# Performance work log

Measured on AMD Instinct MI355X. Metric: run time of the kernel, lower is better.

The kernel has to match this reference:

```python
import jax, jax.numpy as jnp
import numpy as np

NUM_BINS = 8
TAIL_BOUND = 3.0
MIN_V = 1e-3
MIN_DERIV = 1e-3


def _normalize(u):
    # softmax -> min-width floor -> cumsum -> pad left -> map to [-tail, tail]
    v = jax.nn.softmax(u, axis=-1)
    v = MIN_V + (1.0 - MIN_V * NUM_BINS) * v
    cum = jnp.cumsum(v, axis=-1)
    cum = jnp.pad(cum, [(0, 0)] * (cum.ndim - 1) + [(1, 0)])
    return (cum - 0.5) * 2.0 * TAIL_BOUND, v


def _rqs(x_dyn, u_w, u_h, u_d):
    # x_dyn: [B, D]; u_w/u_h: [B, D, K]; u_d: [B, D, K+1]
    cum_w, w = _normalize(u_w)
    cum_h, h = _normalize(u_h)
    d = jax.nn.softplus(u_d) + MIN_DERIV
    cum_w = cum_w.at[..., -1].add(1e-6)  # searchsorted eps on last edge

    idx = jnp.sum((x_dyn[..., None] >= cum_w).astype(jnp.int32), axis=-1) - 1
    idx = jnp.clip(idx, 0, NUM_BINS - 1)[..., None]  # [B, D, 1]

    take = lambda a, i: jnp.take_along_axis(a, i, axis=-1)[..., 0]
    cw, ww = take(cum_w, idx), take(w, idx)
    ch, hh = take(cum_h, idx), take(h, idx)
    di = jnp.clip(take(d, idx), MIN_DERIV, 1000.0)
    di1 = jnp.clip(take(d, idx + 1), MIN_DERIV, 1000.0)

    delta = hh / ww
    theta = jnp.clip((x_dyn - cw) / ww, 0.0, 1.0)
    t1m = theta * (1.0 - theta)
    num_term = di1 * theta ** 2 + delta * t1m
    den = jnp.maximum(delta + (di + di1 - 2.0 * delta) * t1m, 1e-6)
    spline_out = ch + delta * num_term / den * ww
    deriv_num = delta ** 2 * (di1 * theta ** 2 + 2.0 * delta * t1m + di * (1.0 - theta) ** 2)
    spline_logdet = jnp.log(jnp.maximum(deriv_num / den ** 2, 1e-12))

    in_range = (x_dyn >= -TAIL_BOUND) & (x_dyn <= TAIL_BOUND)
    out = jnp.where(in_range, spline_out, x_dyn)
    logdet = jnp.where(in_range, spline_logdet, 0.0)
    return out, logdet


def setup_inputs() -> dict:
    key = jax.random.key(0)
    ks = jax.random.split(key, 3)
    B, D, H = 32768, 128, 256
    total = 3 * NUM_BINS + 1
    x = jax.random.normal(ks[0], (B, D), dtype=jnp.float32)
    mask = (jnp.arange(D) % 2).astype(jnp.float32)
    W1 = jax.random.normal(ks[1], (D, H), dtype=jnp.float32) * (1.0 / np.sqrt(D))
    b1 = jnp.zeros((H,), dtype=jnp.float32)
    W2 = jax.random.normal(ks[2], (H, D * total), dtype=jnp.float32) * (1.0 / np.sqrt(H))
    b2 = jnp.zeros((D * total,), dtype=jnp.float32)
    return {"x": x, "mask": mask, "W1": W1, "b1": b1, "W2": W2, "b2": b2}


def reference(x, mask, W1, b1, W2, b2):
    B, D = x.shape
    total = 3 * NUM_BINS + 1
    x_static = x * mask
    x_dyn = x * (1.0 - mask)
    hidden = jax.nn.relu(x_static @ W1 + b1)
    params = (hidden @ W2 + b2).reshape(B, D, total)
    u_w = params[..., :NUM_BINS]
    u_h = params[..., NUM_BINS:2 * NUM_BINS]
    u_d = params[..., 2 * NUM_BINS:]
    new_dyn, logdet = _rqs(x_dyn, u_w, u_h, u_d)
    out = x_static + new_dyn * (1.0 - mask)
    log_det = jnp.sum(logdet * (1.0 - mask), axis=1)
    return out, log_det
```

## Files before the change

### kernel.cpp

```cpp
#include <hip/hip_runtime.h>
#include <hip/hip_bf16.h>
#include <stdint.h>


#define B_ROWS 32768
#define DDIM   128
#define HDIM   256
#define NPAD   2048
#define LOSCALE 2048.0f
#define INV_LOSCALE (1.0f / 2048.0f)

using f32x4 = __attribute__((ext_vector_type(4))) float;
using f16x8 = __attribute__((ext_vector_type(8))) _Float16;

__device__ __forceinline__ void gl_lds16(const void* g, void* l) {
    __builtin_amdgcn_global_load_lds(
        (__attribute__((address_space(1))) void*)(void*)g,
        (__attribute__((address_space(3))) void*)l, 16, 0, 0);
}

__device__ __forceinline__ float rcpf(float x) { return __builtin_amdgcn_rcpf(x); }

__device__ __forceinline__ float softplus_fast(float z) {
    return fmaxf(z, 0.0f) + __logf(1.0f + __expf(-fabsf(z)));
}

__device__ __forceinline__ void rqs(const float* P, float xv, float& o, float& l) {
    float ew[8], vw[8], edw[9];
    float mw = P[0];
    #pragma unroll
    for (int j = 1; j < 8; ++j) mw = fmaxf(mw, P[j]);
    float sw = 0.0f;
    #pragma unroll
    for (int j = 0; j < 8; ++j) { ew[j] = expf(P[j] - mw); sw += ew[j]; }
    float rsw = rcpf(sw);
    float cum = 0.0f;
    edw[0] = -3.0f;
    #pragma unroll
    for (int j = 0; j < 8; ++j) {
        vw[j] = 0.001f + 0.992f * (ew[j] * rsw);
        cum += vw[j];
        edw[j + 1] = (cum - 0.5f) * 6.0f;
    }
    edw[8] += 1e-6f;

    float eh[8], vh[8], edh[9];
    float mh = P[8];
    #pragma unroll
    for (int j = 1; j < 8; ++j) mh = fmaxf(mh, P[8 + j]);
    float sh = 0.0f;
    #pragma unroll
    for (int j = 0; j < 8; ++j) { eh[j] = expf(P[8 + j] - mh); sh += eh[j]; }
    float rsh = rcpf(sh);
    float cumh = 0.0f;
    edh[0] = -3.0f;
    #pragma unroll
    for (int j = 0; j < 8; ++j) {
        vh[j] = 0.001f + 0.992f * (eh[j] * rsh);
        cumh += vh[j];
        edh[j + 1] = (cumh - 0.5f) * 6.0f;
    }

    float dk[9];
    #pragma unroll
    for (int j = 0; j < 9; ++j) dk[j] = softplus_fast(P[16 + j]) + 0.001f;

    int idx = -1;
    #pragma unroll
    for (int j = 0; j < 9; ++j) idx += (xv >= edw[j]) ? 1 : 0;
    idx = min(max(idx, 0), 7);

    float cw = edw[0], ww = vw[0], ch = edh[0], hh = vh[0], di = dk[0], di1 = dk[1];
    #pragma unroll
    for (int j = 0; j < 8; ++j) {
        bool sel = (idx == j);
        cw  = sel ? edw[j]    : cw;
        ww  = sel ? vw[j]     : ww;
        ch  = sel ? edh[j]    : ch;
        hh  = sel ? vh[j]     : hh;
        di  = sel ? dk[j]     : di;
        di1 = sel ? dk[j + 1] : di1;
    }
    di  = fminf(fmaxf(di,  0.001f), 1000.0f);
    di1 = fminf(fmaxf(di1, 0.001f), 1000.0f);

    float rww   = rcpf(ww);
    float delta = hh * rww;
    float theta = fminf(fmaxf((xv - cw) * rww, 0.0f), 1.0f);
    float t1m   = theta * (1.0f - theta);
    float th2   = theta * theta;
    float omt   = 1.0f - theta;
    float num_term = di1 * th2 + delta * t1m;
    float den      = fmaxf(delta + (di + di1 - 2.0f * delta) * t1m, 1e-6f);
    float rden     = rcpf(den);
    float sp       = ch + delta * num_term * rden * ww;
    float dn       = (delta * delta) * (di1 * th2 + 2.0f * delta * t1m + di * (omt * omt));
    float ld       = __logf(fmaxf(dn * rden * rden, 1e-12f));

    bool inr = (xv >= -3.0f) && (xv <= 3.0f);
    o = inr ? sp : xv;
    l = inr ? ld : 0.0f;
}

__global__ __launch_bounds__(256, 4) void k1_hidden(const float* __restrict__ x,
                                                    const float* __restrict__ W1,
                                                    const float* __restrict__ b1,
                                                    _Float16* __restrict__ hid_hi,
                                                    _Float16* __restrict__ hid_lo,
                                                    float* __restrict__ out,
                                                    float* __restrict__ logdet) {
    __shared__ float xod[32][64];
    const int t  = threadIdx.x;
    const int rb = blockIdx.x * 32;
    #pragma unroll
    for (int u = 0; u < 8; ++u) {
        int idx = u * 256 + t;
        int r = idx >> 6, k = idx & 63;
        float2 v = *(const float2*)&x[(rb + r) * DDIM + 2 * k];
        xod[r][k] = v.y;
        *(float2*)&out[(rb + r) * DDIM + 2 * k] = v;
    }
    if (t < 32) logdet[rb + t] = 0.0f;
    __syncthreads();
    float acc[32];
    #pragma unroll
    for (int r = 0; r < 32; ++r) acc[r] = 0.0f;
    #pragma unroll 2
    for (int k = 0; k < 64; ++k) {
        float w = W1[(2 * k + 1) * HDIM + t];
        #pragma unroll
        for (int r = 0; r < 32; ++r) acc[r] += xod[r][k] * w;
    }
    float bias = b1[t];
    #pragma unroll
    for (int r = 0; r < 32; ++r) {
        float h = fmaxf(acc[r] + bias, 0.0f);
        _Float16 hi = (_Float16)h;
        hid_hi[(rb + r) * HDIM + t] = hi;
        hid_lo[(rb + r) * HDIM + t] = (_Float16)((h - (float)hi) * LOSCALE);
    }
}

__global__ __launch_bounds__(256) void k3_w2split(const float* __restrict__ W2,
                                                  _Float16* __restrict__ w2t_hi,
                                                  _Float16* __restrict__ w2t_lo) {
    int tid = blockIdx.x * 256 + threadIdx.x;
    int n  = tid >> 5;
    int kc = tid & 31;
    int de = n >> 5, j = n & 31;
    f16x8 vh, vl;
    #pragma unroll
    for (int i = 0; i < 8; ++i) {
        float v = (j < 25) ? W2[(size_t)(kc * 8 + i) * 3200 + 50 * de + j] : 0.0f;
        _Float16 h = (_Float16)v;
        vh[i] = h;
        vl[i] = (_Float16)((v - (float)h) * LOSCALE);
    }
    *(f16x8*)&w2t_hi[(size_t)n * HDIM + kc * 8] = vh;
    *(f16x8*)&w2t_lo[(size_t)n * HDIM + kc * 8] = vl;
}

__global__ __launch_bounds__(256, 2) void k2_mfma(
        const float* __restrict__ x,
        const _Float16* __restrict__ hid_hi, const _Float16* __restrict__ hid_lo,
        const _Float16* __restrict__ w2t_hi, const _Float16* __restrict__ w2t_lo,
        const float* __restrict__ b2,
        float* __restrict__ out, float* __restrict__ logdet) {
    __shared__ __align__(16) char smem[128 * 133 * 4];
    const int t    = threadIdx.x;
    const int lane = t & 63;
    const int wave = t >> 6;
    const int m0   = (wave & 1) * 64;
    const int n0   = (wave >> 1) * 64;
    const int row0 = blockIdx.y * 128;
    const int col0 = blockIdx.x * 128;

    f32x4 acc[4][4], acc2[4][4];
    #pragma unroll
    for (int i = 0; i < 4; ++i)
        #pragma unroll
        for (int j = 0; j < 4; ++j) {
            acc[i][j]  = (f32x4){0.f, 0.f, 0.f, 0.f};
            acc2[i][j] = (f32x4){0.f, 0.f, 0.f, 0.f};
        }

    for (int ks = 0; ks < 4; ++ks) {
        __syncthreads();
        #pragma unroll
        for (int call = 0; call < 4; ++call) {
            int g = call * 4 + wave;
            int s = g * 64 + lane;
            int r = s >> 3;
            int c = (s & 7) ^ (r & 7);
            int ke = ks * 64 + c * 8;
            char* ldsb = smem + g * 1024;
            gl_lds16(hid_hi + (size_t)(row0 + r) * HDIM + ke, ldsb);
            gl_lds16(hid_lo + (size_t)(row0 + r) * HDIM + ke, ldsb + 16384);
            gl_lds16(w2t_hi + (size_t)(col0 + r) * HDIM + ke, ldsb + 32768);
            gl_lds16(w2t_lo + (size_t)(col0 + r) * HDIM + ke, ldsb + 49152);
        }
        __syncthreads();
        #pragma unroll
        for (int kk = 0; kk < 2; ++kk) {
            int kc = kk * 4 + (lane >> 4);
            int sw = ((kc ^ (lane & 7)) << 4);
            f16x8 ah[4], al[4], bh[4], bl[4];
            #pragma unroll
            for (int i = 0; i < 4; ++i) {
                int oa = (m0 + i * 16 + (lane & 15)) * 128 + sw;
                ah[i] = *(const f16x8*)(smem + oa);
                al[i] = *(const f16x8*)(smem + 16384 + oa);
                int ob = (n0 + i * 16 + (lane & 15)) * 128 + sw;
                bh[i] = *(const f16x8*)(smem + 32768 + ob);
                bl[i] = *(const f16x8*)(smem + 49152 + ob);
            }
            #pragma unroll
            for (int mi = 0; mi < 4; ++mi)
                #pragma unroll
                for (int ni = 0; ni < 4; ++ni) {
                    acc[mi][ni]  = __builtin_amdgcn_mfma_f32_16x16x32_f16(ah[mi], bh[ni], acc[mi][ni],  0, 0, 0);
                    acc2[mi][ni] = __builtin_amdgcn_mfma_f32_16x16x32_f16(al[mi], bh[ni], acc2[mi][ni], 0, 0, 0);
                    acc2[mi][ni] = __builtin_amdgcn_mfma_f32_16x16x32_f16(ah[mi], bl[ni], acc2[mi][ni], 0, 0, 0);
                }
        }
    }

    __syncthreads();
    float* pf = (float*)smem;
    #pragma unroll
    for (int mi = 0; mi < 4; ++mi)
        #pragma unroll
        for (int ni = 0; ni < 4; ++ni)
            #pragma unroll
            for (int e = 0; e < 4; ++e) {
                int rl = m0 + mi * 16 + (lane >> 4) * 4 + e;
                int cl = n0 + ni * 16 + (lane & 15);
                pf[rl * 133 + cl] = acc[mi][ni][e] + acc2[mi][ni][e] * INV_LOSCALE;
            }
    __syncthreads();

    const int rl   = t & 127;
    const int rowg = blockIdx.y * 128 + rl;
    float ldsum = 0.0f;
    #pragma unroll
    for (int pp = 0; pp < 2; ++pp) {
        int deg = (t >> 7) + 2 * pp;
        int de  = blockIdx.x * 4 + deg;
        float xv = x[(size_t)rowg * DDIM + 2 * de];
        float P[25];
        #pragma unroll
        for (int j = 0; j < 25; ++j)
            P[j] = pf[rl * 133 + deg * 32 + j] + b2[50 * de + j];
        float o, l;
        rqs(P, xv, o, l);
        out[(size_t)rowg * DDIM + 2 * de] = o;
        ldsum += l;
    }
    atomicAdd(&logdet[rowg], ldsum);
}

extern "C" void kernel_launch(void* const* d_in, const int* in_sizes, int n_in,
                              void* d_out, int out_size, void* d_ws, size_t ws_size,
                              hipStream_t stream) {
    const float* x  = (const float*)d_in[0];
    const float* W1 = (const float*)d_in[2];
    const float* b1 = (const float*)d_in[3];
    const float* W2 = (const float*)d_in[4];
    const float* b2 = (const float*)d_in[5];

    float* out    = (float*)d_out;
    float* logdet = (float*)d_out + (size_t)B_ROWS * DDIM;

    _Float16* hid_hi = (_Float16*)d_ws;
    _Float16* hid_lo = hid_hi + (size_t)B_ROWS * HDIM;
    _Float16* w2t_hi = hid_lo + (size_t)B_ROWS * HDIM;
    _Float16* w2t_lo = w2t_hi + (size_t)NPAD * HDIM;

    k3_w2split<<<dim3(NPAD * 32 / 256), dim3(256), 0, stream>>>(W2, w2t_hi, w2t_lo);
    k1_hidden <<<dim3(B_ROWS / 32),     dim3(256), 0, stream>>>(x, W1, b1, hid_hi, hid_lo, out, logdet);
    k2_mfma   <<<dim3(NPAD / 128, B_ROWS / 128), dim3(256), 0, stream>>>(
        x, hid_hi, hid_lo, w2t_hi, w2t_lo, b2, out, logdet);
}
```

Measured before the change: 229.9 us.

## Pack W2 columns densely (5 dims per tile) and register-tile hidden GEMM

The W2 column layout changes from padding each dim's 25 params to 32 to packing 5 dims (125 columns) per 128-column tile. This shrinks the padded N dimension of the main MFMA GEMM from 2048 to 1664 columns and cuts wasted tensor work, and the epilogue is adjusted to process up to 5 dims per block over 3 passes. Separately, the first-layer kernel now uses a transposed LDS tile and an 8x4 register block per thread with float4 loads and vectorized half stores. The risk is an uneven epilogue, where the last pass only half-fills threads and the last tile has partial dims.

```diff
diff --git a/kernel.cpp b/kernel.cpp
--- a/kernel.cpp
+++ b/kernel.cpp
@@ -6,12 +6,13 @@
 #define B_ROWS 32768
 #define DDIM   128
 #define HDIM   256
-#define NPAD   2048
+#define NPACK  1664
 #define LOSCALE 2048.0f
 #define INV_LOSCALE (1.0f / 2048.0f)
 
 using f32x4 = __attribute__((ext_vector_type(4))) float;
 using f16x8 = __attribute__((ext_vector_type(8))) _Float16;
+using f16x4 = __attribute__((ext_vector_type(4))) _Float16;
 
 __device__ __forceinline__ void gl_lds16(const void* g, void* l) {
     __builtin_amdgcn_global_load_lds(
@@ -109,35 +110,56 @@
                                                     _Float16* __restrict__ hid_lo,
                                                     float* __restrict__ out,
                                                     float* __restrict__ logdet) {
-    __shared__ float xod[32][64];
+    __shared__ float xodT[64][36];
     const int t  = threadIdx.x;
     const int rb = blockIdx.x * 32;
+    const int cg = t & 63;
+    const int rg = t >> 6;
     #pragma unroll
     for (int u = 0; u < 8; ++u) {
         int idx = u * 256 + t;
         int r = idx >> 6, k = idx & 63;
         float2 v = *(const float2*)&x[(rb + r) * DDIM + 2 * k];
-        xod[r][k] = v.y;
+        xodT[k][r] = v.y;
         *(float2*)&out[(rb + r) * DDIM + 2 * k] = v;
     }
     if (t < 32) logdet[rb + t] = 0.0f;
     __syncthreads();
-    float acc[32];
-    #pragma unroll
-    for (int r = 0; r < 32; ++r) acc[r] = 0.0f;
-    #pragma unroll 2
+
+    float acc[8][4];
+    #pragma unroll
+    for (int r = 0; r < 8; ++r)
+        #pragma unroll
+        for (int c = 0; c < 4; ++c) acc[r][c] = 0.0f;
+
+    #pragma unroll 4
     for (int k = 0; k < 64; ++k) {
-        float w = W1[(2 * k + 1) * HDIM + t];
-        #pragma unroll
-        for (int r = 0; r < 32; ++r) acc[r] += xod[r][k] * w;
-    }
-    float bias = b1[t];
-    #pragma unroll
-    for (int r = 0; r < 32; ++r) {
-        float h = fmaxf(acc[r] + bias, 0.0f);
-        _Float16 hi = (_Float16)h;
-        hid_hi[(rb + r) * HDIM + t] = hi;
-        hid_lo[(rb + r) * HDIM + t] = (_Float16)((h - (float)hi) * LOSCALE);
+        float4 w  = *(const float4*)&W1[(2 * k + 1) * HDIM + cg * 4];
+        float4 xa = *(const float4*)&xodT[k][rg * 8];
+        float4 xb = *(const float4*)&xodT[k][rg * 8 + 4];
+        float xr[8] = {xa.x, xa.y, xa.z, xa.w, xb.x, xb.y, xb.z, xb.w};
+        float wc[4] = {w.x, w.y, w.z, w.w};
+        #pragma unroll
+        for (int r = 0; r < 8; ++r)
+            #pragma unroll
+            for (int c = 0; c < 4; ++c) acc[r][c] += xr[r] * wc[c];
+    }
+
+    float4 bias = *(const float4*)&b1[cg * 4];
+    float bc[4] = {bias.x, bias.y, bias.z, bias.w};
+    #pragma unroll
+    for (int r = 0; r < 8; ++r) {
+        int row = rb + rg * 8 + r;
+        f16x4 vh, vl;
+        #pragma unroll
+        for (int c = 0; c < 4; ++c) {
+            float h = fmaxf(acc[r][c] + bc[c], 0.0f);
+            _Float16 hi = (_Float16)h;
+            vh[c] = hi;
+            vl[c] = (_Float16)((h - (float)hi) * LOSCALE);
+        }
+        *(f16x4*)&hid_hi[(size_t)row * HDIM + cg * 4] = vh;
+        *(f16x4*)&hid_lo[(size_t)row * HDIM + cg * 4] = vl;
     }
 }
 
@@ -145,19 +167,23 @@
                                                   _Float16* __restrict__ w2t_hi,
                                                   _Float16* __restrict__ w2t_lo) {
     int tid = blockIdx.x * 256 + threadIdx.x;
-    int n  = tid >> 5;
+    int c  = tid >> 5;
     int kc = tid & 31;
-    int de = n >> 5, j = n & 31;
+    int bx = c >> 7;
+    int cb = c & 127;
+    int de = bx * 5 + cb / 25;
+    int j  = cb % 25;
+    bool valid = (cb < 125) && (de < 64);
     f16x8 vh, vl;
     #pragma unroll
     for (int i = 0; i < 8; ++i) {
-        float v = (j < 25) ? W2[(size_t)(kc * 8 + i) * 3200 + 50 * de + j] : 0.0f;
+        float v = valid ? W2[(size_t)(kc * 8 + i) * 3200 + 50 * de + j] : 0.0f;
         _Float16 h = (_Float16)v;
         vh[i] = h;
         vl[i] = (_Float16)((v - (float)h) * LOSCALE);
     }
-    *(f16x8*)&w2t_hi[(size_t)n * HDIM + kc * 8] = vh;
-    *(f16x8*)&w2t_lo[(size_t)n * HDIM + kc * 8] = vl;
+    *(f16x8*)&w2t_hi[(size_t)c * HDIM + kc * 8] = vh;
+    *(f16x8*)&w2t_lo[(size_t)c * HDIM + kc * 8] = vl;
 }
 
 __global__ __launch_bounds__(256, 2) void k2_mfma(
@@ -243,18 +269,20 @@
     const int rowg = blockIdx.y * 128 + rl;
     float ldsum = 0.0f;
     #pragma unroll
-    for (int pp = 0; pp < 2; ++pp) {
-        int deg = (t >> 7) + 2 * pp;
-        int de  = blockIdx.x * 4 + deg;
-        float xv = x[(size_t)rowg * DDIM + 2 * de];
-        float P[25];
-        #pragma unroll
-        for (int j = 0; j < 25; ++j)
-            P[j] = pf[rl * 133 + deg * 32 + j] + b2[50 * de + j];
-        float o, l;
-        rqs(P, xv, o, l);
-        out[(size_t)rowg * DDIM + 2 * de] = o;
-        ldsum += l;
+    for (int pass = 0; pass < 3; ++pass) {
+        int dl = 2 * pass + (t >> 7);
+        int de = blockIdx.x * 5 + dl;
+        if (dl < 5 && de < 64) {
+            float xv = x[(size_t)rowg * DDIM + 2 * de];
+            float P[25];
+            #pragma unroll
+            for (int j = 0; j < 25; ++j)
+                P[j] = pf[rl * 133 + dl * 25 + j] + b2[50 * de + j];
+            float o, l;
+            rqs(P, xv, o, l);
+            out[(size_t)rowg * DDIM + 2 * de] = o;
+            ldsum += l;
+        }
     }
     atomicAdd(&logdet[rowg], ldsum);
 }
@@ -274,10 +302,10 @@
     _Float16* hid_hi = (_Float16*)d_ws;
     _Float16* hid_lo = hid_hi + (size_t)B_ROWS * HDIM;
     _Float16* w2t_hi = hid_lo + (size_t)B_ROWS * HDIM;
-    _Float16* w2t_lo = w2t_hi + (size_t)NPAD * HDIM;
-
-    k3_w2split<<<dim3(NPAD * 32 / 256), dim3(256), 0, stream>>>(W2, w2t_hi, w2t_lo);
-    k1_hidden <<<dim3(B_ROWS / 32),     dim3(256), 0, stream>>>(x, W1, b1, hid_hi, hid_lo, out, logdet);
-    k2_mfma   <<<dim3(NPAD / 128, B_ROWS / 128), dim3(256), 0, stream>>>(
+    _Float16* w2t_lo = w2t_hi + (size_t)NPACK * HDIM;
+
+    k3_w2split<<<dim3(NPACK * 32 / 256), dim3(256), 0, stream>>>(W2, w2t_hi, w2t_lo);
+    k1_hidden <<<dim3(B_ROWS / 32),      dim3(256), 0, stream>>>(x, W1, b1, hid_hi, hid_lo, out, logdet);
+    k2_mfma   <<<dim3(NPACK / 128, B_ROWS / 128), dim3(256), 0, stream>>>(
         x, hid_hi, hid_lo, w2t_hi, w2t_lo, b2, out, logdet);
 }
```

After: 205.2 us. -10.7%, faster.
